# Performance work log

Measured on AMD Instinct MI355X. Metric: run time of the kernel, lower is better.

The kernel has to match this reference:

```python
import jax, jax.numpy as jnp
import numpy as np

EMBED = 1024
HEADS = 16
HEAD_DIM = EMBED // HEADS


def setup_inputs() -> dict:
    key = jax.random.key(0)
    ks = jax.random.split(key, 11)
    N, S = 2, 2048
    scale = 1.0 / np.sqrt(EMBED)
    inp = {
        "values": jax.random.normal(ks[0], (N, S, EMBED), jnp.float32),
        "keys": jax.random.normal(ks[1], (N, S, EMBED), jnp.float32),
        "queries": jax.random.normal(ks[2], (N, S, EMBED), jnp.float32),
        "W_v": jax.random.normal(ks[3], (EMBED, EMBED), jnp.float32) * scale,
        "b_v": jnp.zeros((EMBED,), jnp.float32),
        "W_k": jax.random.normal(ks[4], (EMBED, EMBED), jnp.float32) * scale,
        "b_k": jnp.zeros((EMBED,), jnp.float32),
        "W_q": jax.random.normal(ks[5], (EMBED, EMBED), jnp.float32) * scale,
        "b_q": jnp.zeros((EMBED,), jnp.float32),
        "W_o": jax.random.normal(ks[6], (EMBED, EMBED), jnp.float32) * scale,
        "b_o": jnp.zeros((EMBED,), jnp.float32),
    }
    return inp


def reference(values, keys, queries, W_v, b_v, W_k, b_k, W_q, b_q, W_o, b_o):
    N, q_len, _ = queries.shape
    # linear projections then split heads: [N, S, H, Dh]
    v = (values @ W_v.T + b_v).reshape(N, -1, HEADS, HEAD_DIM)
    k = (keys @ W_k.T + b_k).reshape(N, -1, HEADS, HEAD_DIM)
    q = (queries @ W_q.T + b_q).reshape(N, q_len, HEADS, HEAD_DIM)
    # raw scores [N, H, Q, K]
    energy = jnp.einsum("nqhd,nkhd->nhqk", q, k)
    attention = jax.nn.softmax(energy / np.sqrt(HEAD_DIM), axis=-1)
    out = jnp.einsum("nhql,nlhd->nqhd", attention, v).reshape(N, q_len, EMBED)
    return out @ W_o.T + b_o
```

## Files before the change

### kernel.cpp

```cpp
#include <hip/hip_runtime.h>
#include <hip/hip_bf16.h>


typedef short bf16x8 __attribute__((ext_vector_type(8)));
typedef short bf16x4 __attribute__((ext_vector_type(4)));
typedef float f32x4 __attribute__((ext_vector_type(4)));
typedef float f32x16 __attribute__((ext_vector_type(16)));
typedef unsigned u32x2 __attribute__((ext_vector_type(2)));
typedef unsigned u32x4 __attribute__((ext_vector_type(4)));

constexpr int S = 2048;
constexpr int E = 1024;
constexpr int H = 16;
constexpr int D = 64;
constexpr int M = 2 * S;
#define QSCALE 0.18033688011112042f

static __device__ __forceinline__ short f2bf_rne(float x) {
  unsigned u = __builtin_bit_cast(unsigned, x);
  u += 0x7fff + ((u >> 16) & 1);
  return (short)(u >> 16);
}
static __device__ __forceinline__ bf16x8 cvt8(float4 a, float4 b) {
  bf16x8 t;
  t[0] = f2bf_rne(a.x); t[1] = f2bf_rne(a.y);
  t[2] = f2bf_rne(a.z); t[3] = f2bf_rne(a.w);
  t[4] = f2bf_rne(b.x); t[5] = f2bf_rne(b.y);
  t[6] = f2bf_rne(b.z); t[7] = f2bf_rne(b.w);
  return t;
}
static __device__ __forceinline__ float fast_exp2(float x) {
#if __has_builtin(__builtin_amdgcn_exp2f)
  return __builtin_amdgcn_exp2f(x);
#else
  return __expf(0.69314718055994531f * x);
#endif
}
static __device__ __forceinline__ unsigned cvtpk(float a, float b) {
  unsigned r;
  asm("v_cvt_pk_bf16_f32 %0, %1, %2" : "=v"(r) : "v"(a), "v"(b));
  return r;
}
static __device__ __forceinline__ void plswap(unsigned& a, unsigned& b) {
#if __has_builtin(__builtin_amdgcn_permlane32_swap)
  u32x2 t = __builtin_amdgcn_permlane32_swap(a, b, false, false);
  a = t[0]; b = t[1];
#else
  asm("v_permlane32_swap_b32 %0, %1" : "+v"(a), "+v"(b));
#endif
}

static __device__ __forceinline__ void gl_lds16(const short* g, short* l) {
  __builtin_amdgcn_global_load_lds(
      (const __attribute__((address_space(1))) void*)g,
      (__attribute__((address_space(3))) void*)l, 16, 0, 0);
}


__global__ __launch_bounds__(256) void cast_all(
    const float* __restrict__ qs, const float* __restrict__ ks,
    const float* __restrict__ vsrc, const float* __restrict__ wq,
    const float* __restrict__ wk, const float* __restrict__ wv,
    const float* __restrict__ wo, short* __restrict__ qbf,
    short* __restrict__ kbf, short* __restrict__ vbf, short* __restrict__ wqb,
    short* __restrict__ wkb, short* __restrict__ wvb, short* __restrict__ wob) {
  const float* s;
  short* d;
  switch (blockIdx.y) {
    case 0: s = qs; d = qbf; break;
    case 1: s = ks; d = kbf; break;
    case 2: s = vsrc; d = vbf; break;
    case 3: if (blockIdx.x >= 512) return; s = wq; d = wqb; break;
    case 4: if (blockIdx.x >= 512) return; s = wk; d = wkb; break;
    case 5: if (blockIdx.x >= 512) return; s = wv; d = wvb; break;
    default: if (blockIdx.x >= 512) return; s = wo; d = wob; break;
  }
  size_t i = ((size_t)blockIdx.x * 256 + threadIdx.x) * 8;
  *(bf16x8*)&d[i] = cvt8(*(const float4*)&s[i], *(const float4*)&s[i + 4]);
}

__global__ __launch_bounds__(256) void qk_gemm(
    const short* __restrict__ qbf, const short* __restrict__ kbf,
    const short* __restrict__ wqb, const short* __restrict__ wkb,
    const float* __restrict__ bq, const float* __restrict__ bk,
    short* __restrict__ qb, short* __restrict__ kb) {
  __shared__ __align__(16) short as[128 * 32];
  __shared__ __align__(16) short bs[128 * 32];
  const int tid = threadIdx.x;
  const int lane = tid & 63, w = tid >> 6;
  const int l15 = lane & 15, quad = lane >> 4;
  const int wm = w & 1, wn = w >> 1;

  const int b = blockIdx.x;
  const int c = b & 7, r = b >> 3;
  const int bn = r & 7;
  const int t = c * 8 + (r >> 3);
  const int z = t >> 5, bm = t & 31;

  const short* A = z ? kbf : qbf;
  const short* Bw = z ? wkb : wqb;
  const float* bias = z ? bk : bq;

  const short* agp[2];
  const short* bgp[2];
  int ldsb[2];
#pragma unroll
  for (int cc = 0; cc < 2; ++cc) {
    int seg = w * 2 + cc;
    int p = seg * 8 + (lane >> 3), kc = lane & 7;
    int l = kc ^ (p & 7);
    int row = 2 * p + (l >> 2), col = (l & 3) * 8;
    ldsb[cc] = seg * 512;
    agp[cc] = &A[(size_t)(bm * 128 + row) * E + col];
    bgp[cc] = &Bw[(size_t)(bn * 128 + row) * E + col];
  }

  f32x4 acc[4][4] = {};
  for (int k0 = 0; k0 < E; k0 += 32) {
    __syncthreads();
#pragma unroll
    for (int cc = 0; cc < 2; ++cc) {
      gl_lds16(agp[cc] + k0, &as[ldsb[cc]]);
      gl_lds16(bgp[cc] + k0, &bs[ldsb[cc]]);
    }
    __syncthreads();

    bf16x8 af[4], bf[4];
#pragma unroll
    for (int tt = 0; tt < 4; ++tt) {
      int ra = wm * 64 + tt * 16 + l15;
      int pa2 = ra >> 1, la = (ra & 1) * 4 + quad, ka = la ^ (pa2 & 7);
      af[tt] = *(bf16x8*)&as[pa2 * 64 + ka * 8];
      int rb = wn * 64 + tt * 16 + l15;
      int pb2 = rb >> 1, lb = (rb & 1) * 4 + quad, kb2 = lb ^ (pb2 & 7);
      bf[tt] = *(bf16x8*)&bs[pb2 * 64 + kb2 * 8];
    }
#pragma unroll
    for (int mt = 0; mt < 4; ++mt)
#pragma unroll
      for (int nt = 0; nt < 4; ++nt)
        acc[mt][nt] = __builtin_amdgcn_mfma_f32_16x16x32_bf16(
            af[mt], bf[nt], acc[mt][nt], 0, 0, 0);
  }

#pragma unroll
  for (int mt = 0; mt < 4; ++mt)
#pragma unroll
    for (int nt = 0; nt < 4; ++nt)
#pragma unroll
      for (int rr = 0; rr < 4; ++rr) {
        int row = bm * 128 + wm * 64 + mt * 16 + quad * 4 + rr;
        int col = bn * 128 + wn * 64 + nt * 16 + l15;
        float v = acc[mt][nt][rr] + bias[col];
        int n = row >> 11, s = row & 2047, h = col >> 6, d = col & 63;
        if (z == 0) {
          qb[(((size_t)(n * H + h) * S) + s) * D + d] = f2bf_rne(v * QSCALE);
        } else {
          kb[(((size_t)(n * H + h) * S) + s) * D + d] = f2bf_rne(v);
        }
      }
}

template <int MODE>
__global__ __launch_bounds__(256) void gemm64(const short* __restrict__ A,
                                              const short* __restrict__ Bw,
                                              const float* __restrict__ bias,
                                              void* __restrict__ outp) {
  __shared__ __align__(16) short as[64 * 32];
  __shared__ __align__(16) short bs[128 * 32];
  const int tid = threadIdx.x;
  const int lane = tid & 63, w = tid >> 6;
  const int l15 = lane & 15, quad = lane >> 4;
  const int wm = w & 1, wn = w >> 1;

  const int b = blockIdx.x;
  const int c = b & 7, r = b >> 3;
  const int bn = r & 7;
  const int bm = c * 8 + (r >> 3);

  const short* agp;
  int aldsb;
  {
    int seg = w;
    int p = seg * 8 + (lane >> 3), kc = lane & 7;
    int l = kc ^ (p & 7);
    int row = 2 * p + (l >> 2), col = (l & 3) * 8;
    aldsb = seg * 512;
    agp = &A[(size_t)(bm * 64 + row) * E + col];
  }
  const short* bgp[2];
  int bldsb[2];
#pragma unroll
  for (int cc = 0; cc < 2; ++cc) {
    int seg = w * 2 + cc;
    int p = seg * 8 + (lane >> 3), kc = lane & 7;
    int l = kc ^ (p & 7);
    int row = 2 * p + (l >> 2), col = (l & 3) * 8;
    bldsb[cc] = seg * 512;
    bgp[cc] = &Bw[(size_t)(bn * 128 + row) * E + col];
  }

  f32x4 acc[2][4] = {};
  for (int k0 = 0; k0 < E; k0 += 32) {
    __syncthreads();
    gl_lds16(agp + k0, &as[aldsb]);
#pragma unroll
    for (int cc = 0; cc < 2; ++cc) gl_lds16(bgp[cc] + k0, &bs[bldsb[cc]]);
    __syncthreads();

    bf16x8 af[2], bf[4];
#pragma unroll
    for (int tt = 0; tt < 2; ++tt) {
      int ra = wm * 32 + tt * 16 + l15;
      int pa2 = ra >> 1, la = (ra & 1) * 4 + quad, ka = la ^ (pa2 & 7);
      af[tt] = *(bf16x8*)&as[pa2 * 64 + ka * 8];
    }
#pragma unroll
    for (int tt = 0; tt < 4; ++tt) {
      int rb = wn * 64 + tt * 16 + l15;
      int pb2 = rb >> 1, lb = (rb & 1) * 4 + quad, kb2 = lb ^ (pb2 & 7);
      bf[tt] = *(bf16x8*)&bs[pb2 * 64 + kb2 * 8];
    }
#pragma unroll
    for (int mt = 0; mt < 2; ++mt)
#pragma unroll
      for (int nt = 0; nt < 4; ++nt)
        acc[mt][nt] = __builtin_amdgcn_mfma_f32_16x16x32_bf16(
            af[mt], bf[nt], acc[mt][nt], 0, 0, 0);
  }

#pragma unroll
  for (int mt = 0; mt < 2; ++mt)
#pragma unroll
    for (int nt = 0; nt < 4; ++nt)
#pragma unroll
      for (int rr = 0; rr < 4; ++rr) {
        int row = bm * 64 + wm * 32 + mt * 16 + quad * 4 + rr;
        int col = bn * 128 + wn * 64 + nt * 16 + l15;
        float v = acc[mt][nt][rr] + bias[col];
        if (MODE == 0) {
          int n = row >> 11, s = row & 2047, h = col >> 6, d = col & 63;
          ((short*)outp)[(((size_t)(n * H + h) * D) + d) * S + s] =
              f2bf_rne(v);
        } else {
          ((float*)outp)[(size_t)row * E + col] = v;
        }
      }
}

__global__ __launch_bounds__(512) void attn_kernel(const short* __restrict__ q,
                                                   const short* __restrict__ k,
                                                   const short* __restrict__ vt,
                                                   short* __restrict__ ctx) {
  __shared__ __align__(16) short ksb[2][128 * 72];
  __shared__ __align__(16) short vsb[2][64 * 136];

  const int tid = threadIdx.x;
  const int lane = tid & 63, wv = tid >> 6;
  const int l31 = lane & 31, h = lane >> 5;

  const int bid = blockIdx.y * gridDim.x + blockIdx.x;
  const int c = bid & 7, r = bid >> 3;
  const int qt = r & 7;
  const int hz = c * 4 + (r >> 3);
  const int hh = hz & 15, nn = hz >> 4;

  const size_t base = (size_t)(nn * H + hh) * S * D;
  const int q0 = qt * 256 + wv * 32;

  bf16x8 qf[4];
#pragma unroll
  for (int kd = 0; kd < 4; ++kd)
    qf[kd] = *(const bf16x8*)&q[base + (size_t)(q0 + l31) * D + kd * 16 + h * 8];

  f32x16 o[2] = {};
  float lsum = 0.f;

  bf16x8 pk[2], pv[2];
  auto loadKV = [&](int j0) {
#pragma unroll
    for (int cc = 0; cc < 2; ++cc) {
      int ch = cc * 512 + tid;
      int kr = ch >> 3, kc = (ch & 7) * 8;
      pk[cc] = *(const bf16x8*)&k[base + (size_t)(j0 + kr) * D + kc];
      int vr = ch >> 4, vc = (ch & 15) * 8;
      pv[cc] = *(const bf16x8*)&vt[base + (size_t)vr * S + j0 + vc];
    }
  };
  auto storeKV = [&](int bufi) {
#pragma unroll
    for (int cc = 0; cc < 2; ++cc) {
      int ch = cc * 512 + tid;
      int kr = ch >> 3, kc = (ch & 7) * 8;
      *(bf16x8*)&ksb[bufi][kr * 72 + kc] = pk[cc];
      int vr = ch >> 4, vc = (ch & 15) * 8;
      *(bf16x8*)&vsb[bufi][vr * 136 + vc] = pv[cc];
    }
  };

  loadKV(0);
  storeKV(0);
  loadKV(128);
  __syncthreads();

  for (int t = 0; t < 16; ++t) {
    const int cur = t & 1;
    if (t + 1 < 16) storeKV(cur ^ 1);
    if (t + 2 < 16) loadKV((t + 2) * 128);
    const short* ks = ksb[cur];
    const short* vs = vsb[cur];

#pragma unroll
    for (int half = 0; half < 2; ++half) {
      f32x16 sc[2] = {};
      __builtin_amdgcn_s_setprio(1);
#pragma unroll
      for (int c2 = 0; c2 < 2; ++c2)
#pragma unroll
        for (int kd = 0; kd < 4; ++kd) {
          bf16x8 kf = *(bf16x8*)&ks[(half * 64 + c2 * 32 + l31) * 72 +
                                    kd * 16 + h * 8];
          sc[c2] = __builtin_amdgcn_mfma_f32_32x32x16_bf16(kf, qf[kd], sc[c2],
                                                           0, 0, 0);
        }
      __builtin_amdgcn_s_setprio(0);

      bf16x8 pa[4];
#pragma unroll
      for (int c2 = 0; c2 < 2; ++c2) {
        float pe[16];
#pragma unroll
        for (int rr = 0; rr < 16; ++rr) {
          float p = fast_exp2(sc[c2][rr]);
          lsum += p;
          pe[rr] = p;
        }
#pragma unroll
        for (int kk = 0; kk < 2; ++kk) {
          unsigned A0 = cvtpk(pe[8 * kk + 0], pe[8 * kk + 1]);
          unsigned A1 = cvtpk(pe[8 * kk + 2], pe[8 * kk + 3]);
          unsigned B0 = cvtpk(pe[8 * kk + 4], pe[8 * kk + 5]);
          unsigned B1 = cvtpk(pe[8 * kk + 6], pe[8 * kk + 7]);
          plswap(A0, B0);
          plswap(A1, B1);
          u32x4 tt;
          tt[0] = A0; tt[1] = A1; tt[2] = B0; tt[3] = B1;
          pa[c2 * 2 + kk] = __builtin_bit_cast(bf16x8, tt);
        }
      }

      __builtin_amdgcn_s_setprio(1);
#pragma unroll
      for (int ks2 = 0; ks2 < 4; ++ks2)
#pragma unroll
        for (int dc = 0; dc < 2; ++dc) {
          bf16x8 vf = *(bf16x8*)&vs[(dc * 32 + l31) * 136 + half * 64 +
                                    ks2 * 16 + h * 8];
          o[dc] = __builtin_amdgcn_mfma_f32_32x32x16_bf16(pa[ks2], vf, o[dc],
                                                          0, 0, 0);
        }
      __builtin_amdgcn_s_setprio(0);
    }
    __syncthreads();
  }

  lsum += __shfl_xor(lsum, 32);
  float invq = 1.0f / lsum;

#pragma unroll
  for (int rr = 0; rr < 16; ++rr) {
    int crow = (rr & 3) + 8 * (rr >> 2) + 4 * h;
    float inv = __shfl(invq, crow);
    int row = q0 + crow;
#pragma unroll
    for (int dc = 0; dc < 2; ++dc) {
      ctx[((size_t)(nn * S + row)) * E + hh * D + dc * 32 + l31] =
          f2bf_rne(o[dc][rr] * inv);
    }
  }
}

extern "C" void kernel_launch(void* const* d_in, const int* in_sizes, int n_in,
                              void* d_out, int out_size, void* d_ws,
                              size_t ws_size, hipStream_t stream) {
  const float* values  = (const float*)d_in[0];
  const float* keys    = (const float*)d_in[1];
  const float* queries = (const float*)d_in[2];
  const float* b_v = (const float*)d_in[4];
  const float* b_k = (const float*)d_in[6];
  const float* b_q = (const float*)d_in[8];
  const float* W_v = (const float*)d_in[3];
  const float* W_k = (const float*)d_in[5];
  const float* W_q = (const float*)d_in[7];
  const float* W_o = (const float*)d_in[9];
  const float* b_o = (const float*)d_in[10];

  const size_t X = (size_t)M * E;
  const size_t W = (size_t)E * E;

  short* qbf = (short*)d_out;
  short* qb  = (short*)d_out + X;
  short* kbf = (short*)d_ws;
  short* vbf = kbf + X;
  short* vtb = vbf + X;
  short* wqb = vtb + X;
  short* wkb = wqb + W;
  short* wvb = wkb + W;
  short* wob = wvb + W;
  short* ctx = kbf;
  short* kb  = vbf;

  cast_all<<<dim3(2048, 7), 256, 0, stream>>>(queries, keys, values, W_q, W_k,
                                              W_v, W_o, qbf, kbf, vbf, wqb,
                                              wkb, wvb, wob);
  gemm64<0><<<512, 256, 0, stream>>>(vbf, wvb, b_v, vtb);
  qk_gemm<<<512, 256, 0, stream>>>(qbf, kbf, wqb, wkb, b_q, b_k, qb, kb);
  attn_kernel<<<dim3(8, 32), 512, 0, stream>>>(qb, kb, vtb, ctx);
  gemm64<1><<<512, 256, 0, stream>>>(ctx, wob, b_o, d_out);
}
```

Before: 211.5 us.

## Use 128x128 GEMM tiles and compute softmax row sums via MFMA

```diff
diff --git a/kernel.cpp b/kernel.cpp
--- a/kernel.cpp
+++ b/kernel.cpp
@@ -162,50 +162,39 @@
 }
 
 template <int MODE>
-__global__ __launch_bounds__(256) void gemm64(const short* __restrict__ A,
-                                              const short* __restrict__ Bw,
-                                              const float* __restrict__ bias,
-                                              void* __restrict__ outp) {
-  __shared__ __align__(16) short as[64 * 32];
+__global__ __launch_bounds__(512) void gemm128(const short* __restrict__ A,
+                                               const short* __restrict__ Bw,
+                                               const float* __restrict__ bias,
+                                               void* __restrict__ outp) {
+  __shared__ __align__(16) short as[128 * 32];
   __shared__ __align__(16) short bs[128 * 32];
   const int tid = threadIdx.x;
   const int lane = tid & 63, w = tid >> 6;
   const int l15 = lane & 15, quad = lane >> 4;
-  const int wm = w & 1, wn = w >> 1;
+  const int wm = w & 3, wn = w >> 2;
 
   const int b = blockIdx.x;
   const int c = b & 7, r = b >> 3;
-  const int bn = r & 7;
-  const int bm = c * 8 + (r >> 3);
+  const int t = c * 32 + r;
+  const int bm = t >> 3, bn = t & 7;
 
   const short* agp;
-  int aldsb;
+  const short* bgp;
+  int ldsb;
   {
-    int seg = w;
-    int p = seg * 8 + (lane >> 3), kc = lane & 7;
+    int p = w * 8 + (lane >> 3), kc = lane & 7;
     int l = kc ^ (p & 7);
     int row = 2 * p + (l >> 2), col = (l & 3) * 8;
-    aldsb = seg * 512;
-    agp = &A[(size_t)(bm * 64 + row) * E + col];
-  }
-  const short* bgp[2];
-  int bldsb[2];
-#pragma unroll
-  for (int cc = 0; cc < 2; ++cc) {
-    int seg = w * 2 + cc;
-    int p = seg * 8 + (lane >> 3), kc = lane & 7;
-    int l = kc ^ (p & 7);
-    int row = 2 * p + (l >> 2), col = (l & 3) * 8;
-    bldsb[cc] = seg * 512;
-    bgp[cc] = &Bw[(size_t)(bn * 128 + row) * E + col];
+    ldsb = w * 512;
+    agp = &A[(size_t)(bm * 128 + row) * E + col];
+    bgp = &Bw[(size_t)(bn * 128 + row) * E + col];
   }
 
   f32x4 acc[2][4] = {};
   for (int k0 = 0; k0 < E; k0 += 32) {
     __syncthreads();
-    gl_lds16(agp + k0, &as[aldsb]);
-#pragma unroll
-    for (int cc = 0; cc < 2; ++cc) gl_lds16(bgp[cc] + k0, &bs[bldsb[cc]]);
+    gl_lds16(agp + k0, &as[ldsb]);
+    gl_lds16(bgp + k0, &bs[ldsb]);
     __syncthreads();
 
     bf16x8 af[2], bf[4];
@@ -235,7 +224,7 @@
     for (int nt = 0; nt < 4; ++nt)
 #pragma unroll
       for (int rr = 0; rr < 4; ++rr) {
-        int row = bm * 64 + wm * 32 + mt * 16 + quad * 4 + rr;
+        int row = bm * 128 + wm * 32 + mt * 16 + quad * 4 + rr;
         int col = bn * 128 + wn * 64 + nt * 16 + l15;
         float v = acc[mt][nt][rr] + bias[col];
         if (MODE == 0) {
@@ -274,7 +263,9 @@
     qf[kd] = *(const bf16x8*)&q[base + (size_t)(q0 + l31) * D + kd * 16 + h * 8];
 
   f32x16 o[2] = {};
-  float lsum = 0.f;
+  f32x16 oS = {};
+  const bf16x8 vone = {0x3F80, 0x3F80, 0x3F80, 0x3F80,
+                       0x3F80, 0x3F80, 0x3F80, 0x3F80};
 
   bf16x8 pk[2], pv[2];
   auto loadKV = [&](int j0) {
@@ -330,11 +321,7 @@
       for (int c2 = 0; c2 < 2; ++c2) {
         float pe[16];
 #pragma unroll
-        for (int rr = 0; rr < 16; ++rr) {
-          float p = fast_exp2(sc[c2][rr]);
-          lsum += p;
-          pe[rr] = p;
-        }
+        for (int rr = 0; rr < 16; ++rr) pe[rr] = fast_exp2(sc[c2][rr]);
 #pragma unroll
         for (int kk = 0; kk < 2; ++kk) {
           unsigned A0 = cvtpk(pe[8 * kk + 0], pe[8 * kk + 1]);
@@ -351,7 +338,7 @@
 
       __builtin_amdgcn_s_setprio(1);
 #pragma unroll
-      for (int ks2 = 0; ks2 < 4; ++ks2)
+      for (int ks2 = 0; ks2 < 4; ++ks2) {
 #pragma unroll
         for (int dc = 0; dc < 2; ++dc) {
           bf16x8 vf = *(bf16x8*)&vs[(dc * 32 + l31) * 136 + half * 64 +
@@ -359,18 +346,18 @@
           o[dc] = __builtin_amdgcn_mfma_f32_32x32x16_bf16(pa[ks2], vf, o[dc],
                                                           0, 0, 0);
         }
+        oS = __builtin_amdgcn_mfma_f32_32x32x16_bf16(pa[ks2], vone, oS,
+                                                     0, 0, 0);
+      }
       __builtin_amdgcn_s_setprio(0);
     }
     __syncthreads();
   }
 
-  lsum += __shfl_xor(lsum, 32);
-  float invq = 1.0f / lsum;
-
 #pragma unroll
   for (int rr = 0; rr < 16; ++rr) {
+    float inv = 1.0f / oS[rr];
     int crow = (rr & 3) + 8 * (rr >> 2) + 4 * h;
-    float inv = __shfl(invq, crow);
     int row = q0 + crow;
 #pragma unroll
     for (int dc = 0; dc < 2; ++dc) {
@@ -413,8 +400,8 @@
   cast_all<<<dim3(2048, 7), 256, 0, stream>>>(queries, keys, values, W_q, W_k,
                                               W_v, W_o, qbf, kbf, vbf, wqb,
                                               wkb, wvb, wob);
-  gemm64<0><<<512, 256, 0, stream>>>(vbf, wvb, b_v, vtb);
+  gemm128<0><<<256, 512, 0, stream>>>(vbf, wvb, b_v, vtb);
   qk_gemm<<<512, 256, 0, stream>>>(qbf, kbf, wqb, wkb, b_q, b_k, qb, kb);
   attn_kernel<<<dim3(8, 32), 512, 0, stream>>>(qb, kb, vtb, ctx);
-  gemm64<1><<<512, 256, 0, stream>>>(ctx, wob, b_o, d_out);
-}
+  gemm128<1><<<256, 512, 0, stream>>>(ctx, wob, b_o, d_out);
+}
```

Result: slower. 216.5 us (+2.4%).
